# Kernel tuning notes

Hardware: AMD Instinct MI355X
Metric: run time of the kernel (lower is better)

The kernel has to match this reference:

```python
import jax, jax.numpy as jnp
import numpy as np

F_NHID = 64
C_NHID = 64
U_INIT = F_NHID + C_NHID + 1   # 129
U_OUT = F_NHID + C_NHID        # 128
U_HID = 128
N_AGG = 4
M_INIT = 3 * N_AGG * U_OUT + C_NHID  # 1600
M_HID = 256
M_OUT = C_NHID


def setup_inputs() -> dict:
    key = jax.random.key(0)
    ks = jax.random.split(key, 12)
    B, Nc, Nf = 4, 512, 256
    h_fac = jax.random.normal(ks[0], (B, Nf, F_NHID), dtype=jnp.float32)
    h_cus = jax.random.normal(ks[1], (B, Nc, C_NHID), dtype=jnp.float32)
    edge = jax.random.normal(ks[2], (B, Nc, Nf, 1), dtype=jnp.float32)
    adj = jax.random.randint(ks[3], (B, Nc, Nf), 0, 2).astype(jnp.float32)
    def lin(k, i, o):
        return jax.random.normal(k, (i, o), dtype=jnp.float32) / np.sqrt(i)
    return {
        'h_fac': h_fac, 'h_cus': h_cus, 'edge': edge, 'adj': adj,
        'U_W1': lin(ks[4], U_INIT, U_HID), 'U_b1': jnp.zeros((U_HID,), jnp.float32),
        'U_W2': lin(ks[5], U_HID, U_OUT), 'U_b2': jnp.zeros((U_OUT,), jnp.float32),
        'M_W1': lin(ks[6], M_INIT, M_HID), 'M_b1': jnp.zeros((M_HID,), jnp.float32),
        'M_W2': lin(ks[7], M_HID, M_OUT), 'M_b2': jnp.zeros((M_OUT,), jnp.float32),
    }


def reference(h_fac, h_cus, edge, adj, U_W1, U_b1, U_W2, U_b2, M_W1, M_b1, M_W2, M_b2):
    B, Nc, c = h_cus.shape
    Nf = h_fac.shape[1]
    # Per-edge message input: [customer_feat, facility_feat, edge_scalar] -> (B,Nc,Nf,U_INIT)
    msg = jnp.concatenate([
        jnp.broadcast_to(h_cus[:, :, None, :], (B, Nc, Nf, c)),
        jnp.broadcast_to(h_fac[:, None, :, :], (B, Nc, Nf, h_fac.shape[-1])),
        edge,
    ], axis=-1)
    # U MLP (pretransformation): relu -> linear
    m = jax.nn.relu(msg @ U_W1 + U_b1)
    m = m @ U_W2 + U_b2  # (B, Nc, Nf, U_OUT)

    mask = adj > 0                              # (B, Nc, Nf)
    maskf = mask[..., None].astype(m.dtype)     # (B, Nc, Nf, 1)
    cnt = jnp.sum(maskf, axis=2)                # (B, Nc, 1)
    mean = jnp.sum(m * maskf, axis=2) / cnt     # nanmean over masked entries
    var = jnp.sum(((m - mean[:, :, None, :]) ** 2) * maskf, axis=2) / cnt
    std = jnp.sqrt(var)                         # population std (divides by count)
    mx = jnp.max(jnp.where(mask[..., None], m, -jnp.inf), axis=2)
    mn = jnp.min(jnp.where(mask[..., None], m, jnp.inf), axis=2)

    # Degree-based scalers (get_avgd + scale_amplification/attenuation)
    deg_c = jnp.sum(adj, axis=-1)               # (B, Nc)
    deg_f = jnp.sum(adj, axis=-2)               # (B, Nf)
    avg_d = jnp.mean(jnp.concatenate([jnp.log(deg_c + 1.0), jnp.log(deg_f + 1.0)], axis=-1), axis=-1)  # (B,)
    scale = (jnp.log(deg_c + 1.0) / avg_d[:, None])[..., None]          # (B, Nc, 1)
    scale_inv = jnp.where(scale != 0, 1.0 / scale, jnp.zeros_like(scale))

    feats = [h_cus]
    for a in (mean, std, mx, mn):
        feats.extend([a, a * scale, a * scale_inv])
    h = jnp.concatenate(feats, axis=-1)         # (B, Nc, M_INIT)

    # M MLP (posttransformation): relu -> linear (last activation 'none')
    h = jax.nn.relu(h @ M_W1 + M_b1)
    out = h @ M_W2 + M_b2                       # (B, Nc, C_NHID)
    return out
```

## Files before the change

kernel.cpp:

```cpp
#include <hip/hip_runtime.h>
#include <hip/hip_bf16.h>


using bs8 = __attribute__((ext_vector_type(8))) short;
using f4  = __attribute__((ext_vector_type(4))) float;
using f2  = __attribute__((ext_vector_type(2))) float;

__device__ __forceinline__ unsigned short f2bf(float f) {
    union { float f; unsigned int u; } x; x.f = f;
    unsigned int u = x.u + 0x7FFFu + ((x.u >> 16) & 1u);
    return (unsigned short)(u >> 16);
}

__device__ __forceinline__ unsigned int pkbf(float a, float b) {
    __hip_bfloat162 h = __float22bfloat162_rn(make_float2(a, b));
    union { __hip_bfloat162 h; unsigned int u; } c; c.h = h;
    return c.u;
}

__global__ void PNALayer_35081292874189_kernel() {}

#define OFF_AC     0u
#define OFF_AF     1048576u
#define OFF_DEGC   1572864u
#define OFF_DEGF   1581056u
#define OFF_SCALE  1585152u
#define OFF_SINV   1593344u
#define OFF_FEATB  1601536u
#define OFF_HMID   8155392u
#define OFF_W2T    10252544u
#define OFF_W1TB   10318080u
#define WS_NEED    11170048u

__global__ void PNALayer_ws_fail(float* out, int n) {
    int i = blockIdx.x * 256 + threadIdx.x;
    if (i < n) out[i] = 2500.0f;
}

__global__ void PNALayer_prep1(
    const float* h_fac, const float* h_cus, const float* adj,
    const float* U_W1, const float* U_b1, const float* U_W2, const float* M_W1,
    float* wsAc, float* wsAf, float* wsDegC, float* wsDegF,
    unsigned short* wsW2Tb, unsigned short* wsW1Tb)
{
    __shared__ float sH[64];
    __shared__ float sRed[256];
    __shared__ float sT[64][65];
    int bid = blockIdx.x, t = threadIdx.x;

    if (bid < 1024) {
        int b = bid >> 8, f = bid & 255;
        if (t < 64) sH[t] = h_fac[(b * 256 + f) * 64 + t];
        __syncthreads();
        if (t < 128) {
            float acc = 0.f;
            for (int k = 0; k < 64; ++k)
                acc += sH[k] * U_W1[(64 + k) * 128 + t];
            wsAf[(b * 256 + f) * 128 + t] = acc;
        }
        float v = adj[(b * 512 + t) * 256 + f] + adj[(b * 512 + t + 256) * 256 + f];
        sRed[t] = v; __syncthreads();
        for (int s = 128; s > 0; s >>= 1) { if (t < s) sRed[t] += sRed[t + s]; __syncthreads(); }
        if (t == 0) wsDegF[b * 256 + f] = sRed[0];
    } else if (bid < 3072) {
        int bc = bid - 1024;
        if (t < 64) sH[t] = h_cus[bc * 64 + t];
        __syncthreads();
        if (t < 128) {
            float acc = U_b1[t];
            for (int k = 0; k < 64; ++k)
                acc += sH[k] * U_W1[k * 128 + t];
            wsAc[bc * 128 + t] = acc;
        }
        float v = adj[bc * 256 + t];
        sRed[t] = v; __syncthreads();
        for (int s = 128; s > 0; s >>= 1) { if (t < s) sRed[t] += sRed[t + s]; __syncthreads(); }
        if (t == 0) wsDegC[bc] = sRed[0];
    } else if (bid < 3076) {
        int l = bid - 3072;
        int k0 = (l >> 1) * 64, n0 = (l & 1) * 64;
        for (int rep = 0; rep < 16; ++rep) {
            int idx = rep * 256 + t; int r = idx >> 6, c = idx & 63;
            sT[r][c] = U_W2[(k0 + r) * 128 + n0 + c];
        }
        __syncthreads();
        for (int rep = 0; rep < 16; ++rep) {
            int idx = rep * 256 + t; int r = idx >> 6, c = idx & 63;
            wsW2Tb[(n0 + r) * 128 + k0 + c] = f2bf(sT[c][r]);
        }
    } else if (bid < 3176) {
        int l = bid - 3076;
        int k0 = (l % 25) * 64, n0 = (l / 25) * 64;
        for (int rep = 0; rep < 16; ++rep) {
            int idx = rep * 256 + t; int r = idx >> 6, c = idx & 63;
            sT[r][c] = M_W1[(k0 + r) * 256 + n0 + c];
        }
        __syncthreads();
        for (int rep = 0; rep < 16; ++rep) {
            int idx = rep * 256 + t; int r = idx >> 6, c = idx & 63;
            wsW1Tb[(n0 + r) * 1664 + k0 + c] = f2bf(sT[c][r]);
        }
    } else {
        for (int i = 0; i < 64; ++i) {
            int idx = i * 256 + t;
            int n = idx >> 6, k = 1600 + (idx & 63);
            wsW1Tb[n * 1664 + k] = 0;
        }
    }
}

__global__ void PNALayer_prep2(
    const float* wsDegC, const float* wsDegF, float* wsScale, float* wsSinv)
{
    __shared__ float sRed[256];
    __shared__ float sAvg;
    int b = blockIdx.x, t = threadIdx.x;
    float v = logf(wsDegC[b * 512 + t] + 1.f) + logf(wsDegC[b * 512 + t + 256] + 1.f)
            + logf(wsDegF[b * 256 + t] + 1.f);
    sRed[t] = v; __syncthreads();
    for (int s = 128; s > 0; s >>= 1) { if (t < s) sRed[t] += sRed[t + s]; __syncthreads(); }
    if (t == 0) sAvg = sRed[0] / 768.f;
    __syncthreads();
    float avg = sAvg;
    for (int c = t; c < 512; c += 256) {
        float lg = logf(wsDegC[b * 512 + c] + 1.f);
        float sc = lg / avg;
        float si = (sc != 0.f) ? 1.f / sc : 0.f;
        wsScale[b * 512 + c] = sc;
        wsSinv[b * 512 + c] = si;
    }
}

__global__ __launch_bounds__(512, 6) void PNALayer_edge(
    const float* h_cus, const float* edge, const float* adj,
    const float* U_W1, const float* U_b2,
    const float* wsAc, const float* wsAf, const unsigned short* wsW2Tb,
    const float* wsDegC, const float* wsScale, const float* wsSinv,
    unsigned short* featB)
{
    __shared__ __align__(16) unsigned short sM1[64 * 136];
    __shared__ float sE[256];
    __shared__ float sMk[256];
    __shared__ float sAc[128];
    __shared__ float sWe[128];

    int bc = blockIdx.x;
    int b  = bc >> 9;
    int t  = threadIdx.x;
    int w = t >> 6, quad = (t >> 4) & 3, ln = t & 15;

    int r0 = w * 16 + ln;
    bs8 bw[4];
#pragma unroll
    for (int kk = 0; kk < 4; ++kk)
        bw[kk] = *(const bs8*)(wsW2Tb + r0 * 128 + kk * 32 + quad * 8);
    float b2v = U_b2[r0];

    if (t < 256) {
        sE[t]  = edge[bc * 256 + t];
        sMk[t] = (adj[bc * 256 + t] > 0.f) ? 1.f : 0.f;
    }
    if (t < 128) {
        sAc[t] = wsAc[bc * 128 + t];
        sWe[t] = U_W1[128 * 128 + t];
    }
    if (t >= 128 && t < 192) {
        int j = t - 128;
        featB[bc * 1600 + j] = f2bf(h_cus[bc * 64 + j]);
    }
    __syncthreads();

    float aS = 0.f, aQ = 0.f, aMx = -1e30f, aMn = 1e30f;
    const f2 zero2 = (f2){0.f, 0.f};

    for (int ft = 0; ft < 4; ++ft) {
#pragma unroll
        for (int i = 0; i < 4; ++i) {
            int idx = i * 512 + t;
            int fl = idx >> 5, k = (idx & 31) * 4;
            int f = ft * 64 + fl;
            float4 af  = *(const float4*)(wsAf + (b * 256 + f) * 128 + k);
            f2 ac01 = *(const f2*)(sAc + k);
            f2 ac23 = *(const f2*)(sAc + k + 2);
            f2 we01 = *(const f2*)(sWe + k);
            f2 we23 = *(const f2*)(sWe + k + 2);
            float e = sE[f];
            f2 e2 = (f2){e, e};
            f2 s01 = ac01 + (f2){af.x, af.y};
            f2 s23 = ac23 + (f2){af.z, af.w};
            s01 = __builtin_elementwise_fma(e2, we01, s01);
            s23 = __builtin_elementwise_fma(e2, we23, s23);
            f2 r01 = __builtin_elementwise_max(s01, zero2);
            f2 r23 = __builtin_elementwise_max(s23, zero2);
            uint2 p;
            p.x = pkbf(r01.x, r01.y);
            p.y = pkbf(r23.x, r23.y);
            *(uint2*)(sM1 + fl * 136 + k) = p;
        }
        __syncthreads();

        f4 acc[4];
#pragma unroll
        for (int rt = 0; rt < 4; ++rt) acc[rt] = (f4){0.f, 0.f, 0.f, 0.f};
#pragma unroll
        for (int kk = 0; kk < 4; ++kk) {
            int ko = kk * 32 + quad * 8;
#pragma unroll
            for (int rt = 0; rt < 4; ++rt) {
                bs8 a = *(const bs8*)(sM1 + (rt * 16 + ln) * 136 + ko);
                acc[rt] = __builtin_amdgcn_mfma_f32_16x16x32_bf16(a, bw[kk], acc[rt], 0, 0, 0);
            }
        }

#pragma unroll
        for (int rt = 0; rt < 4; ++rt) {
#pragma unroll
            for (int i = 0; i < 4; ++i) {
                int f = ft * 64 + rt * 16 + quad * 4 + i;
                if (sMk[f] > 0.f) {
                    float v = acc[rt][i];
                    aS += v;
                    aQ = fmaf(v, v, aQ);
                    aMx = fmaxf(aMx, v);
                    aMn = fminf(aMn, v);
                }
            }
        }
        __syncthreads();
    }

    aS  += __shfl_xor(aS, 16, 64);  aS  += __shfl_xor(aS, 32, 64);
    aQ  += __shfl_xor(aQ, 16, 64);  aQ  += __shfl_xor(aQ, 32, 64);
    aMx = fmaxf(aMx, __shfl_xor(aMx, 16, 64));
    aMx = fmaxf(aMx, __shfl_xor(aMx, 32, 64));
    aMn = fminf(aMn, __shfl_xor(aMn, 16, 64));
    aMn = fminf(aMn, __shfl_xor(aMn, 32, 64));

    if (quad == 0) {
        float cnt = wsDegC[bc];
        float sc = wsScale[bc], si = wsSinv[bc];
        unsigned short* fr = featB + bc * 1600;
        int col = w * 16 + ln;
        float meanr = aS / cnt;
        float mean  = meanr + b2v;
        float var   = fmaxf(aQ / cnt - meanr * meanr, 0.f);
        float stdv  = sqrtf(var);
        float mx = aMx + b2v, mn = aMn + b2v;
        fr[64 + col]   = f2bf(mean); fr[192 + col]  = f2bf(mean * sc); fr[320 + col]  = f2bf(mean * si);
        fr[448 + col]  = f2bf(stdv); fr[576 + col]  = f2bf(stdv * sc); fr[704 + col]  = f2bf(stdv * si);
        fr[832 + col]  = f2bf(mx);   fr[960 + col]  = f2bf(mx * sc);   fr[1088 + col] = f2bf(mx * si);
        fr[1216 + col] = f2bf(mn);   fr[1344 + col] = f2bf(mn * sc);   fr[1472 + col] = f2bf(mn * si);
    }
}

__global__ __launch_bounds__(256) void PNALayer_mlp1(
    const unsigned short* featB, const unsigned short* wsW1Tb, const float* M_b1,
    float* h_mid)
{
    __shared__ __align__(16) unsigned short sA[64 * 136];
    __shared__ __align__(16) unsigned short sB[64 * 136];
    int t = threadIdx.x;
    int rb = (blockIdx.x >> 2) * 64, cb = (blockIdx.x & 3) * 64;
    int w = t >> 6, quad = (t >> 4) & 3, ln = t & 15;

    f4 acc[4];
#pragma unroll
    for (int rt = 0; rt < 4; ++rt) acc[rt] = (f4){0.f, 0.f, 0.f, 0.f};

    for (int kt = 0; kt < 13; ++kt) {
        int kb = kt * 128;
#pragma unroll
        for (int i = 0; i < 4; ++i) {
            int vi = i * 256 + t;
            int row = vi >> 4, c8 = (vi & 15) * 8;
            *(uint4*)(sA + row * 136 + c8) =
                *(const uint4*)(featB + (rb + row) * 1600 + kb + c8);
        }
#pragma unroll
        for (int i = 0; i < 4; ++i) {
            int vi = i * 256 + t;
            int row = vi >> 4, c8 = (vi & 15) * 8;
            *(uint4*)(sB + row * 136 + c8) =
                *(const uint4*)(wsW1Tb + (cb + row) * 1664 + kb + c8);
        }
        __syncthreads();
#pragma unroll
        for (int kk = 0; kk < 4; ++kk) {
            int ko = kk * 32 + quad * 8;
            bs8 bb = *(const bs8*)(sB + (w * 16 + ln) * 136 + ko);
#pragma unroll
            for (int rt = 0; rt < 4; ++rt) {
                bs8 a = *(const bs8*)(sA + (rt * 16 + ln) * 136 + ko);
                acc[rt] = __builtin_amdgcn_mfma_f32_16x16x32_bf16(a, bb, acc[rt], 0, 0, 0);
            }
        }
        __syncthreads();
    }
    int col = cb + w * 16 + ln;
    float b1v = M_b1[col];
#pragma unroll
    for (int rt = 0; rt < 4; ++rt) {
#pragma unroll
        for (int i = 0; i < 4; ++i) {
            int row = rb + rt * 16 + quad * 4 + i;
            h_mid[row * 256 + col] = fmaxf(acc[rt][i] + b1v, 0.f);
        }
    }
}

__global__ void PNALayer_mlp2(
    const float* h_mid, const float* M_W2, const float* M_b2, float* out)
{
    int idx = blockIdx.x * 256 + threadIdx.x;
    int row = idx >> 6, j = idx & 63;
    float acc = M_b2[j];
    const float* hr = h_mid + row * 256;
#pragma unroll 8
    for (int k = 0; k < 256; ++k)
        acc += hr[k] * M_W2[k * 64 + j];
    out[idx] = acc;
}

extern "C" void kernel_launch(void* const* d_in, const int* in_sizes, int n_in,
                              void* d_out, int out_size, void* d_ws, size_t ws_size,
                              hipStream_t stream) {
    const float* h_fac = (const float*)d_in[0];
    const float* h_cus = (const float*)d_in[1];
    const float* edge  = (const float*)d_in[2];
    const float* adj   = (const float*)d_in[3];
    const float* U_W1  = (const float*)d_in[4];
    const float* U_b1  = (const float*)d_in[5];
    const float* U_W2  = (const float*)d_in[6];
    const float* U_b2  = (const float*)d_in[7];
    const float* M_W1  = (const float*)d_in[8];
    const float* M_b1  = (const float*)d_in[9];
    const float* M_W2  = (const float*)d_in[10];
    const float* M_b2  = (const float*)d_in[11];
    (void)in_sizes; (void)n_in;

    float* outp = (float*)d_out;
    int nblk_out = (out_size + 255) / 256;

    if (ws_size < (size_t)WS_NEED) {
        PNALayer_ws_fail<<<nblk_out, 256, 0, stream>>>(outp, out_size);
        return;
    }

    char* ws = (char*)d_ws;
    float*          wsAc   = (float*)(ws + OFF_AC);
    float*          wsAf   = (float*)(ws + OFF_AF);
    float*          wsDegC = (float*)(ws + OFF_DEGC);
    float*          wsDegF = (float*)(ws + OFF_DEGF);
    float*          wsScal = (float*)(ws + OFF_SCALE);
    float*          wsSinv = (float*)(ws + OFF_SINV);
    unsigned short* wsFeatB= (unsigned short*)(ws + OFF_FEATB);
    float*          wsHmid = (float*)(ws + OFF_HMID);
    unsigned short* wsW2Tb = (unsigned short*)(ws + OFF_W2T);
    unsigned short* wsW1Tb = (unsigned short*)(ws + OFF_W1TB);

    PNALayer_prep1<<<3177, 256, 0, stream>>>(
        h_fac, h_cus, adj, U_W1, U_b1, U_W2, M_W1,
        wsAc, wsAf, wsDegC, wsDegF, wsW2Tb, wsW1Tb);
    PNALayer_prep2<<<4, 256, 0, stream>>>(wsDegC, wsDegF, wsScal, wsSinv);
    PNALayer_edge<<<2048, 512, 0, stream>>>(
        h_cus, edge, adj, U_W1, U_b2,
        wsAc, wsAf, wsW2Tb, wsDegC, wsScal, wsSinv, wsFeatB);
    PNALayer_mlp1<<<128, 256, 0, stream>>>(wsFeatB, wsW1Tb, M_b1, wsHmid);
    PNALayer_mlp2<<<512, 256, 0, stream>>>(wsHmid, M_W2, M_b2, outp);
}
```

Baseline: 159.9 us.

## Compact masked facilities per customer and shrink MLP1 row tiles for more blocks

The edge kernel builds a ballot-based compacted list of facility indices where adj is set, then runs the U-MLP only over tiles of selected edges instead of all 256. With roughly half the edges masked, this should cut the MFMA and load work about in half, and the count now comes from the popcount instead of the degree buffer. MLP1 switches from 64-row to 16-row tiles, launching 512 blocks instead of 128 to fill more compute units, at the cost of re-reading the weight tiles more often.

```diff
diff --git a/kernel.cpp b/kernel.cpp
--- a/kernel.cpp
+++ b/kernel.cpp
@@ -135,14 +135,15 @@
     const float* h_cus, const float* edge, const float* adj,
     const float* U_W1, const float* U_b2,
     const float* wsAc, const float* wsAf, const unsigned short* wsW2Tb,
-    const float* wsDegC, const float* wsScale, const float* wsSinv,
+    const float* wsScale, const float* wsSinv,
     unsigned short* featB)
 {
     __shared__ __align__(16) unsigned short sM1[64 * 136];
     __shared__ float sE[256];
-    __shared__ float sMk[256];
     __shared__ float sAc[128];
     __shared__ float sWe[128];
+    __shared__ unsigned short sFidx[256];
+    __shared__ unsigned long long sBal[4];
 
     int bc = blockIdx.x;
     int b  = bc >> 9;
@@ -156,45 +157,68 @@
         bw[kk] = *(const bs8*)(wsW2Tb + r0 * 128 + kk * 32 + quad * 8);
     float b2v = U_b2[r0];
 
+    bool m = false;
+    unsigned long long bal = 0;
     if (t < 256) {
-        sE[t]  = edge[bc * 256 + t];
-        sMk[t] = (adj[bc * 256 + t] > 0.f) ? 1.f : 0.f;
-    }
-    if (t < 128) {
-        sAc[t] = wsAc[bc * 128 + t];
-        sWe[t] = U_W1[128 * 128 + t];
-    }
-    if (t >= 128 && t < 192) {
-        int j = t - 128;
+        sE[t] = edge[bc * 256 + t];
+        m = adj[bc * 256 + t] > 0.f;
+        bal = __ballot(m);
+        if ((t & 63) == 0) sBal[t >> 6] = bal;
+    }
+    if (t >= 256 && t < 384) {
+        int j = t - 256;
+        sAc[j] = wsAc[bc * 128 + j];
+        sWe[j] = U_W1[128 * 128 + j];
+    }
+    if (t >= 384 && t < 448) {
+        int j = t - 384;
         featB[bc * 1600 + j] = f2bf(h_cus[bc * 64 + j]);
     }
     __syncthreads();
+
+    unsigned long long b0 = sBal[0], b1 = sBal[1], b2 = sBal[2], b3 = sBal[3];
+    int cnt = __popcll(b0) + __popcll(b1) + __popcll(b2) + __popcll(b3);
+    if (t < 256) {
+        int wv = t >> 6, l = t & 63;
+        int base = 0;
+        if (wv > 0) base += __popcll(b0);
+        if (wv > 1) base += __popcll(b1);
+        if (wv > 2) base += __popcll(b2);
+        int rank = __popcll(bal & ((1ULL << l) - 1ULL));
+        if (m) sFidx[base + rank] = (unsigned short)t;
+    }
+    __syncthreads();
+
+    int ntiles = (cnt + 63) >> 6;
 
     float aS = 0.f, aQ = 0.f, aMx = -1e30f, aMn = 1e30f;
     const f2 zero2 = (f2){0.f, 0.f};
 
-    for (int ft = 0; ft < 4; ++ft) {
+    for (int tl = 0; tl < ntiles; ++tl) {
 #pragma unroll
         for (int i = 0; i < 4; ++i) {
             int idx = i * 512 + t;
             int fl = idx >> 5, k = (idx & 31) * 4;
-            int f = ft * 64 + fl;
-            float4 af  = *(const float4*)(wsAf + (b * 256 + f) * 128 + k);
-            f2 ac01 = *(const f2*)(sAc + k);
-            f2 ac23 = *(const f2*)(sAc + k + 2);
-            f2 we01 = *(const f2*)(sWe + k);
-            f2 we23 = *(const f2*)(sWe + k + 2);
-            float e = sE[f];
-            f2 e2 = (f2){e, e};
-            f2 s01 = ac01 + (f2){af.x, af.y};
-            f2 s23 = ac23 + (f2){af.z, af.w};
-            s01 = __builtin_elementwise_fma(e2, we01, s01);
-            s23 = __builtin_elementwise_fma(e2, we23, s23);
-            f2 r01 = __builtin_elementwise_max(s01, zero2);
-            f2 r23 = __builtin_elementwise_max(s23, zero2);
-            uint2 p;
-            p.x = pkbf(r01.x, r01.y);
-            p.y = pkbf(r23.x, r23.y);
+            int fj = tl * 64 + fl;
+            uint2 p = make_uint2(0u, 0u);
+            if (fj < cnt) {
+                int f = sFidx[fj];
+                float4 af  = *(const float4*)(wsAf + (b * 256 + f) * 128 + k);
+                f2 ac01 = *(const f2*)(sAc + k);
+                f2 ac23 = *(const f2*)(sAc + k + 2);
+                f2 we01 = *(const f2*)(sWe + k);
+                f2 we23 = *(const f2*)(sWe + k + 2);
+                float e = sE[f];
+                f2 e2 = (f2){e, e};
+                f2 s01 = ac01 + (f2){af.x, af.y};
+                f2 s23 = ac23 + (f2){af.z, af.w};
+                s01 = __builtin_elementwise_fma(e2, we01, s01);
+                s23 = __builtin_elementwise_fma(e2, we23, s23);
+                f2 r01 = __builtin_elementwise_max(s01, zero2);
+                f2 r23 = __builtin_elementwise_max(s23, zero2);
+                p.x = pkbf(r01.x, r01.y);
+                p.y = pkbf(r23.x, r23.y);
+            }
             *(uint2*)(sM1 + fl * 136 + k) = p;
         }
         __syncthreads();
@@ -216,8 +240,8 @@
         for (int rt = 0; rt < 4; ++rt) {
 #pragma unroll
             for (int i = 0; i < 4; ++i) {
-                int f = ft * 64 + rt * 16 + quad * 4 + i;
-                if (sMk[f] > 0.f) {
+                int fj = tl * 64 + rt * 16 + quad * 4 + i;
+                if (fj < cnt) {
                     float v = acc[rt][i];
                     aS += v;
                     aQ = fmaf(v, v, aQ);
@@ -237,13 +261,13 @@
     aMn = fminf(aMn, __shfl_xor(aMn, 32, 64));
 
     if (quad == 0) {
-        float cnt = wsDegC[bc];
+        float cntf = (float)cnt;
         float sc = wsScale[bc], si = wsSinv[bc];
         unsigned short* fr = featB + bc * 1600;
         int col = w * 16 + ln;
-        float meanr = aS / cnt;
+        float meanr = aS / cntf;
         float mean  = meanr + b2v;
-        float var   = fmaxf(aQ / cnt - meanr * meanr, 0.f);
+        float var   = fmaxf(aQ / cntf - meanr * meanr, 0.f);
         float stdv  = sqrtf(var);
         float mx = aMx + b2v, mn = aMn + b2v;
         fr[64 + col]   = f2bf(mean); fr[192 + col]  = f2bf(mean * sc); fr[320 + col]  = f2bf(mean * si);
@@ -257,26 +281,21 @@
     const unsigned short* featB, const unsigned short* wsW1Tb, const float* M_b1,
     float* h_mid)
 {
-    __shared__ __align__(16) unsigned short sA[64 * 136];
+    __shared__ __align__(16) unsigned short sA[16 * 136];
     __shared__ __align__(16) unsigned short sB[64 * 136];
     int t = threadIdx.x;
-    int rb = (blockIdx.x >> 2) * 64, cb = (blockIdx.x & 3) * 64;
+    int rb = (blockIdx.x >> 2) * 16, cb = (blockIdx.x & 3) * 64;
     int w = t >> 6, quad = (t >> 4) & 3, ln = t & 15;
 
-    f4 acc[4];
-#pragma unroll
-    for (int rt = 0; rt < 4; ++rt) acc[rt] = (f4){0.f, 0.f, 0.f, 0.f};
+    f4 acc = (f4){0.f, 0.f, 0.f, 0.f};
 
     for (int kt = 0; kt < 13; ++kt) {
         int kb = kt * 128;
-#pragma unroll
-        for (int i = 0; i < 4; ++i) {
-            int vi = i * 256 + t;
-            int row = vi >> 4, c8 = (vi & 15) * 8;
+        {
+            int row = t >> 4, c8 = (t & 15) * 8;
             *(uint4*)(sA + row * 136 + c8) =
                 *(const uint4*)(featB + (rb + row) * 1600 + kb + c8);
         }
-#pragma unroll
         for (int i = 0; i < 4; ++i) {
             int vi = i * 256 + t;
             int row = vi >> 4, c8 = (vi & 15) * 8;
@@ -284,27 +303,19 @@
                 *(const uint4*)(wsW1Tb + (cb + row) * 1664 + kb + c8);
         }
         __syncthreads();
-#pragma unroll
         for (int kk = 0; kk < 4; ++kk) {
             int ko = kk * 32 + quad * 8;
+            bs8 a = *(const bs8*)(sA + ln * 136 + ko);
             bs8 bb = *(const bs8*)(sB + (w * 16 + ln) * 136 + ko);
-#pragma unroll
-            for (int rt = 0; rt < 4; ++rt) {
-                bs8 a = *(const bs8*)(sA + (rt * 16 + ln) * 136 + ko);
-                acc[rt] = __builtin_amdgcn_mfma_f32_16x16x32_bf16(a, bb, acc[rt], 0, 0, 0);
-            }
+            acc = __builtin_amdgcn_mfma_f32_16x16x32_bf16(a, bb, acc, 0, 0, 0);
         }
         __syncthreads();
     }
     int col = cb + w * 16 + ln;
     float b1v = M_b1[col];
-#pragma unroll
-    for (int rt = 0; rt < 4; ++rt) {
-#pragma unroll
-        for (int i = 0; i < 4; ++i) {
-            int row = rb + rt * 16 + quad * 4 + i;
-            h_mid[row * 256 + col] = fmaxf(acc[rt][i] + b1v, 0.f);
-        }
+    for (int i = 0; i < 4; ++i) {
+        int row = rb + quad * 4 + i;
+        h_mid[row * 256 + col] = fmaxf(acc[i] + b1v, 0.f);
     }
 }
 
@@ -364,7 +375,7 @@
     PNALayer_prep2<<<4, 256, 0, stream>>>(wsDegC, wsDegF, wsScal, wsSinv);
     PNALayer_edge<<<2048, 512, 0, stream>>>(
         h_cus, edge, adj, U_W1, U_b2,
-        wsAc, wsAf, wsW2Tb, wsDegC, wsScal, wsSinv, wsFeatB);
-    PNALayer_mlp1<<<128, 256, 0, stream>>>(wsFeatB, wsW1Tb, M_b1, wsHmid);
+        wsAc, wsAf, wsW2Tb, wsScal, wsSinv, wsFeatB);
+    PNALayer_mlp1<<<512, 256, 0, stream>>>(wsFeatB, wsW1Tb, M_b1, wsHmid);
     PNALayer_mlp2<<<512, 256, 0, stream>>>(wsHmid, M_W2, M_b2, outp);
 }
```

New measurement: 149.3 us. 1.07x faster.
